# Performance work log

Measured on AMD Instinct MI355X. Metric: run time of the kernel, lower is better.

## Reference

```python
import jax, jax.numpy as jnp
import numpy as np

B, C, H, W = 32, 512, 32, 32
N = H * W            # seq_len = 1024
HEADS = 8
DH = C // HEADS      # 64
K = 256              # linformer low-rank
EPS = 1e-5


def setup_inputs() -> dict:
    key = jax.random.key(0)
    ks = jax.random.split(key, 10)
    s = 0.02
    return {
        "x": jax.random.normal(ks[0], (B, C, H, W), dtype=jnp.float32),
        "pos": jax.random.normal(ks[1], (1, N, C), dtype=jnp.float32),
        "ln_g": jnp.ones((C,), dtype=jnp.float32),
        "ln_b": jnp.zeros((C,), dtype=jnp.float32),
        "Wq": jax.random.normal(ks[2], (C, C), dtype=jnp.float32) * s,
        "Wk": jax.random.normal(ks[3], (C, C), dtype=jnp.float32) * s,
        "Wv": jax.random.normal(ks[4], (C, C), dtype=jnp.float32) * s,
        "proj_k": jax.random.normal(ks[5], (N, K), dtype=jnp.float32) * s,
        "proj_v": jax.random.normal(ks[6], (N, K), dtype=jnp.float32) * s,
        "Wo": jax.random.normal(ks[7], (C, C), dtype=jnp.float32) * s,
        "bo": jnp.zeros((C,), dtype=jnp.float32),
    }


def reference(x, pos, ln_g, ln_b, Wq, Wk, Wv, proj_k, proj_v, Wo, bo):
    b, c, h, w = x.shape
    n = h * w
    # b c h w -> b (h w) c
    xf = x.reshape(b, c, n).transpose(0, 2, 1) + pos
    # LayerNorm (biased variance, eps=1e-5) + ReLU; dropout = identity (eval)
    mu = xf.mean(-1, keepdims=True)
    var = jnp.var(xf, axis=-1, keepdims=True)
    y = (xf - mu) * jax.lax.rsqrt(var + EPS) * ln_g + ln_b
    y = jax.nn.relu(y)
    # Linformer self-attention
    q = y @ Wq                                   # [b,n,c]
    k_ = jnp.einsum('bnd,nk->bkd', y @ Wk, proj_k)  # [b,K,c]
    v_ = jnp.einsum('bnd,nk->bkd', y @ Wv, proj_v)  # [b,K,c]
    q = q.reshape(b, n, HEADS, DH)
    k_ = k_.reshape(b, K, HEADS, DH)
    v_ = v_.reshape(b, K, HEADS, DH)
    dots = jnp.einsum('bnhd,bkhd->bhnk', q, k_) * (DH ** -0.5)
    attn = jax.nn.softmax(dots, axis=-1)
    out = jnp.einsum('bhnk,bkhd->bnhd', attn, v_).reshape(b, n, c)
    out = out @ Wo + bo
    # residual with (x + pos), then back to b c h w
    out = out + xf
    return out.transpose(0, 2, 1).reshape(b, c, h, w)
```

## Files before the change

### kernel.cpp

```cpp
#include <hip/hip_runtime.h>
#include <hip/hip_bf16.h>
#include <cstdint>

#define BB  32
#define CC  512
#define NN  1024
#define HH  8
#define DHH 64
#define KR  256

using f32x4  = __attribute__((ext_vector_type(4))) float;
using f32x16 = __attribute__((ext_vector_type(16))) float;
using bf16x8 = __attribute__((ext_vector_type(8))) __bf16;
using u32x4  = __attribute__((ext_vector_type(4))) unsigned int;

__device__ __forceinline__ unsigned short f2bf(float f) {
  unsigned int u = __float_as_uint(f);
  u += 0x7fffu + ((u >> 16) & 1u);
  return (unsigned short)(u >> 16);
}

__device__ __forceinline__ float bf2f(unsigned short u) {
  return __uint_as_float(((unsigned int)u) << 16);
}

__device__ __forceinline__ unsigned int pknat(float a, float b) {
  unsigned short ua = __builtin_bit_cast(unsigned short, (__bf16)a);
  unsigned short ub = __builtin_bit_cast(unsigned short, (__bf16)b);
  return (unsigned int)ua | ((unsigned int)ub << 16);
}

__device__ __forceinline__ void gload16(const void* gsrc, void* ldst) {
  __builtin_amdgcn_global_load_lds(
      (const __attribute__((address_space(1))) unsigned int*)gsrc,
      (__attribute__((address_space(3))) unsigned int*)ldst, 16, 0, 0);
}

__global__ __launch_bounds__(256) void transcvt_all(
    const float* __restrict__ w0, const float* __restrict__ w1,
    const float* __restrict__ w2, const float* __restrict__ w3,
    const float* __restrict__ p0, const float* __restrict__ p1,
    const float* __restrict__ pos,
    unsigned short* __restrict__ d0, unsigned short* __restrict__ d1,
    unsigned short* __restrict__ d2, unsigned short* __restrict__ d3,
    unsigned short* __restrict__ e0, unsigned short* __restrict__ e1,
    float* __restrict__ posT) {
  const int m = blockIdx.y;
  int idx = blockIdx.x * 256 + threadIdx.x;
  if (m == 6) {
    #pragma unroll
    for (int h = 0; h < 2; ++h) {
      int e = idx + h * 262144;
      int c = e >> 10, n = e & 1023;
      posT[e] = pos[(size_t)n * CC + c];
    }
    return;
  }
  const float* src = m==0?w0:m==1?w1:m==2?w2:m==3?w3:m==4?p0:p1;
  unsigned short* dst = m==0?d0:m==1?d1:m==2?d2:m==3?d3:m==4?e0:e1;
  if (m < 4) {
    int dr = idx & 511;
    int dc = idx >> 9;
    dst[idx] = f2bf(src[(size_t)dr * 512 + dc]);
  } else {
    int n = idx & 1023, kk = idx >> 10;
    dst[idx] = f2bf(src[(size_t)n * 256 + kk]);
  }
}

__global__ __launch_bounds__(1024) void ln_relu_kernel(
    const float* __restrict__ x, const float* __restrict__ posT,
    const float* __restrict__ g, const float* __restrict__ bta,
    unsigned short* __restrict__ y, unsigned short* __restrict__ yT) {
  __shared__ unsigned short tile[512][68];
  __shared__ float smp[16][16][8];
  __shared__ float smu[64], srs[64];
  const int b = blockIdx.y, n0 = blockIdx.x * 64;
  const int tid = threadIdx.x;
  const int wv = tid >> 6, ln_ = tid & 63;
  const int q = tid & 15;
  const int rr = tid >> 4;
  const float* xb = x    + (size_t)b * CC * NN + n0 + q * 4;
  const float* pb = posT + n0 + q * 4;

  float4 xf[8];
  float s[4] = {0.f,0.f,0.f,0.f}, s2[4] = {0.f,0.f,0.f,0.f};
  #pragma unroll
  for (int hh = 0; hh < 2; ++hh) {
    float4 xv[4], pv[4];
    #pragma unroll
    for (int i = 0; i < 4; ++i) {
      const int c = rr + (hh * 4 + i) * 64;
      xv[i] = *reinterpret_cast<const float4*>(&xb[(size_t)c * NN]);
      pv[i] = *reinterpret_cast<const float4*>(&pb[(size_t)c * NN]);
    }
    #pragma unroll
    for (int i = 0; i < 4; ++i) {
      float4 f;
      f.x = xv[i].x + pv[i].x; f.y = xv[i].y + pv[i].y;
      f.z = xv[i].z + pv[i].z; f.w = xv[i].w + pv[i].w;
      s[0] += f.x; s2[0] += f.x * f.x;
      s[1] += f.y; s2[1] += f.y * f.y;
      s[2] += f.z; s2[2] += f.z * f.z;
      s[3] += f.w; s2[3] += f.w * f.w;
      xf[hh * 4 + i] = f;
    }
  }
  #pragma unroll
  for (int d = 16; d < 64; d <<= 1)
    #pragma unroll
    for (int k = 0; k < 4; ++k) {
      s[k]  += __shfl_xor(s[k],  d, 64);
      s2[k] += __shfl_xor(s2[k], d, 64);
    }
  if (ln_ < 16) {
    #pragma unroll
    for (int k = 0; k < 4; ++k) {
      smp[wv][ln_][k]     = s[k];
      smp[wv][ln_][k + 4] = s2[k];
    }
  }
  __syncthreads();

  if (tid < 64) {
    const int qq = tid >> 2, k = tid & 3;
    float ss = 0.f, ss2 = 0.f;
    #pragma unroll
    for (int w = 0; w < 16; ++w) { ss += smp[w][qq][k]; ss2 += smp[w][qq][k + 4]; }
    float mu = ss * (1.f / 512.f);
    float var = ss2 * (1.f / 512.f) - mu * mu;
    smu[tid] = mu;
    srs[tid] = rsqrtf(var + 1e-5f);
  }
  __syncthreads();

  {
    const float mu0 = smu[q * 4 + 0], rs0 = srs[q * 4 + 0];
    const float mu1 = smu[q * 4 + 1], rs1 = srs[q * 4 + 1];
    const float mu2 = smu[q * 4 + 2], rs2 = srs[q * 4 + 2];
    const float mu3 = smu[q * 4 + 3], rs3 = srs[q * 4 + 3];
    #pragma unroll
    for (int i = 0; i < 8; ++i) {
      const int c = rr + i * 64;
      const float gg = g[c], bb = bta[c];
      float o0 = (xf[i].x - mu0) * rs0 * gg + bb; o0 = o0 > 0.f ? o0 : 0.f;
      float o1 = (xf[i].y - mu1) * rs1 * gg + bb; o1 = o1 > 0.f ? o1 : 0.f;
      float o2 = (xf[i].z - mu2) * rs2 * gg + bb; o2 = o2 > 0.f ? o2 : 0.f;
      float o3 = (xf[i].w - mu3) * rs3 * gg + bb; o3 = o3 > 0.f ? o3 : 0.f;
      uint2 u; u.x = pknat(o0, o1); u.y = pknat(o2, o3);
      *reinterpret_cast<uint2*>(&tile[c][q * 4]) = u;
    }
  }
  __syncthreads();

  {
    const int tok = tid >> 4, seg = tid & 15;
    const int c0 = seg * 32;
    unsigned int pk16[16];
    #pragma unroll
    for (int cc = 0; cc < 32; cc += 2) {
      const int ccr = (cc + seg * 2) & 31;
      unsigned short v0 = tile[c0 + ccr][tok];
      unsigned short v1 = tile[c0 + ccr + 1][tok];
      pk16[ccr >> 1] = (unsigned int)v0 | ((unsigned int)v1 << 16);
    }
    unsigned short* yb = y + ((size_t)b * NN + n0 + tok) * CC + c0;
    #pragma unroll
    for (int v4 = 0; v4 < 4; ++v4) {
      uint4 w;
      w.x = pk16[v4 * 4 + 0]; w.y = pk16[v4 * 4 + 1];
      w.z = pk16[v4 * 4 + 2]; w.w = pk16[v4 * 4 + 3];
      *reinterpret_cast<uint4*>(&yb[v4 * 8]) = w;
    }
  }

  {
    const int c = tid & 511, hf = tid >> 9;
    const int toff = hf * 32;
    unsigned short* ytb = yT + (size_t)b * CC * NN + (size_t)c * NN + n0 + toff;
    #pragma unroll
    for (int v4 = 0; v4 < 4; ++v4) {
      uint2 a0 = *reinterpret_cast<const uint2*>(&tile[c][toff + v4 * 8]);
      uint2 a1 = *reinterpret_cast<const uint2*>(&tile[c][toff + v4 * 8 + 4]);
      uint4 w; w.x = a0.x; w.y = a0.y; w.z = a1.x; w.w = a1.y;
      *reinterpret_cast<uint4*>(&ytb[v4 * 8]) = w;
    }
  }
}

template <int MODE>
__global__ __launch_bounds__(256) void gemm_tn(
    const unsigned short* __restrict__ A, int lda, long long strideA,
    const unsigned short* __restrict__ Bt, int ldb, long long strideB,
    unsigned short* __restrict__ Cb, long long strideC,
    unsigned short* __restrict__ Cb2, long long strideC2,
    int Nn, int Kk, int TB,
    const float* __restrict__ xres, const float* __restrict__ posT,
    const float* __restrict__ bias, float* __restrict__ outF) {
  __shared__ __align__(16) unsigned short sh[24576];
  unsigned short* aL = sh;
  unsigned short* bL = sh + 12288;
  const int zb = blockIdx.z;
  int sel = 0, mb;
  if (MODE == 3) {
    sel = blockIdx.y >> 1;
    mb = ((blockIdx.y & 1) + sel * 2) * 128;
    if (sel == 1) Bt += (size_t)512 * 512;
  } else {
    mb = blockIdx.y * 128;
  }
  const int nb = blockIdx.x * 128;
  A  += (size_t)strideA * zb;
  Bt += (size_t)strideB * zb;
  Cb += (size_t)strideC * zb;
  if (MODE == 3) Cb2 += (size_t)strideC2 * zb;
  const int tid  = threadIdx.x;
  const int lane = tid & 63;
  const int wave = tid >> 6;
  const int wm = (wave >> 1) * 64, wn = (wave & 1) * 64;
  const int sr  = lane >> 2;
  const int scw = lane & 3;
  f32x4 acc[4][4] = {};

  auto stage = [&](int buf, int k0) {
    #pragma unroll
    for (int i = 0; i < 2; ++i) {
      int rbase = wave * 32 + i * 16;
      int row = rbase + sr;
      int ca = scw ^ ((row ^ (row >> 2)) & 3);
      gload16(&A [(size_t)(mb + row) * lda + k0 + ca * 8], &aL[buf * 4096 + rbase * 32]);
      gload16(&Bt[(size_t)(nb + row) * ldb + k0 + ca * 8], &bL[buf * 4096 + rbase * 32]);
    }
  };

  const int nt = Kk >> 5;
  stage(0, 0);
  stage(1, 32);
  asm volatile("s_waitcnt vmcnt(4)" ::: "memory");
  __builtin_amdgcn_s_barrier();
  __builtin_amdgcn_sched_barrier(0);

  int cbuf = 0;
  for (int t = 0; t < nt; ++t) {
    if (t + 2 < nt) stage(cbuf == 0 ? 2 : cbuf - 1, (t + 2) << 5);

    bf16x8 af[4], bfv[4];
    const int kc = lane >> 4;
    #pragma unroll
    for (int i = 0; i < 4; ++i) {
      int ra = wm + i * 16 + (lane & 15);
      int rb = wn + i * 16 + (lane & 15);
      af[i]  = *reinterpret_cast<const bf16x8*>(&aL[cbuf * 4096 + ra * 32 + (kc ^ ((ra ^ (ra >> 2)) & 3)) * 8]);
      bfv[i] = *reinterpret_cast<const bf16x8*>(&bL[cbuf * 4096 + rb * 32 + (kc ^ ((rb ^ (rb >> 2)) & 3)) * 8]);
    }
    #pragma unroll
    for (int i = 0; i < 4; ++i)
      #pragma unroll
      for (int j = 0; j < 4; ++j)
        acc[i][j] = __builtin_amdgcn_mfma_f32_16x16x32_bf16(af[i], bfv[j], acc[i][j], 0, 0, 0);

    if (t + 2 < nt)      { asm volatile("s_waitcnt vmcnt(4)" ::: "memory"); }
    else if (t + 1 < nt) { asm volatile("s_waitcnt vmcnt(0)" ::: "memory"); }
    if (t + 1 < nt) {
      __builtin_amdgcn_s_barrier();
      __builtin_amdgcn_sched_barrier(0);
    }
    cbuf = (cbuf == 2) ? 0 : cbuf + 1;
  }

  if (MODE == 2) {
    float* Ct = reinterpret_cast<float*>(sh);
    const int halfsel = wave >> 1;
    const int t0base = nb & 1023;
    const int bcell = nb >> 10;
    float4 xr[16];
    #pragma unroll
    for (int half = 0; half < 2; ++half)
      #pragma unroll
      for (int p8 = 0; p8 < 8; ++p8) {
        int e = p8 * 256 + tid;
        int r = e >> 5, f4 = (e & 31) * 4;
        int c = mb + half * 64 + r;
        xr[half * 8 + p8] = *reinterpret_cast<const float4*>(
            &xres[((size_t)bcell * CC + c) * NN + t0base + f4]);
      }
    #pragma unroll
    for (int half = 0; half < 2; ++half) {
      __syncthreads();
      if (halfsel == half) {
        #pragma unroll
        for (int i = 0; i < 4; ++i) {
          int rloc = i * 16 + ((lane >> 4) << 2);
          #pragma unroll
          for (int j = 0; j < 4; ++j) {
            int cl = wn + j * 16 + (lane & 15);
            #pragma unroll
            for (int t = 0; t < 4; ++t)
              Ct[(rloc + t) * 132 + cl] = acc[i][j][t];
          }
        }
      }
      __syncthreads();
      #pragma unroll
      for (int p8 = 0; p8 < 8; ++p8) {
        int e = p8 * 256 + tid;
        int r = e >> 5, f4 = (e & 31) * 4;
        int c = mb + half * 64 + r;
        size_t base = ((size_t)bcell * CC + c) * NN + t0base + f4;
        float4 cv = *reinterpret_cast<const float4*>(&Ct[r * 132 + f4]);
        float4 xv = xr[half * 8 + p8];
        float4 pv = *reinterpret_cast<const float4*>(&posT[(size_t)c * NN + t0base + f4]);
        float bc = bias[c];
        float4 ov;
        ov.x = cv.x + xv.x + pv.x + bc;
        ov.y = cv.y + xv.y + pv.y + bc;
        ov.z = cv.z + xv.z + pv.z + bc;
        ov.w = cv.w + xv.w + pv.w + bc;
        *reinterpret_cast<float4*>(&outF[base]) = ov;
      }
    }
  } else {
    const bool transp = (MODE == 1) || (MODE == 3 && sel == 1);
    auto Ct = (unsigned short (*)[136])sh;
    __syncthreads();
    #pragma unroll
    for (int i = 0; i < 4; ++i) {
      const int r0 = wm + i * 16 + ((lane >> 4) << 2);
      #pragma unroll
      for (int j = 0; j < 4; ++j) {
        const int cl = wn + j * 16 + (lane & 15);
        #pragma unroll
        for (int t = 0; t < 4; ++t) {
          if (!transp) Ct[r0 + t][cl] = f2bf(acc[i][j][t]);
          else         Ct[cl][r0 + t] = f2bf(acc[i][j][t]);
        }
      }
    }
    __syncthreads();
    const int rr = tid >> 4, ch = tid & 15;
    #pragma unroll
    for (int it = 0; it < 8; ++it) {
      const int r = it * 16 + rr;
      uint4 v = *reinterpret_cast<const uint4*>(&Ct[r][ch * 8]);
      if (!transp)
        *reinterpret_cast<uint4*>(&Cb[(size_t)(mb + r) * Nn + nb + ch * 8]) = v;
      else if (MODE == 1)
        *reinterpret_cast<uint4*>(&Cb[(size_t)(nb + r) * TB + mb + ch * 8]) = v;
      else
        *reinterpret_cast<uint4*>(&Cb2[(size_t)(nb + r) * TB + (mb - 256) + ch * 8]) = v;
    }
  }
}

__global__ __launch_bounds__(256, 2) void attn_kernel(
    const unsigned short* __restrict__ q,
    const unsigned short* __restrict__ kB,
    const unsigned short* __restrict__ vT,
    unsigned short* __restrict__ O) {
  __shared__ __align__(16) unsigned short smem[32768];
  const int wgid = blockIdx.x;
  const int grp  = wgid & 255;
  const int tg   = wgid >> 8;
  const int h = grp & 7, b = grp >> 3;
  const int wave = threadIdx.x >> 6, lane = threadIdx.x & 63;
  const int t32 = lane & 31, g2 = lane >> 5;
  const int tokb = tg * 128 + wave * 32;

  const unsigned short* qp = q + ((size_t)(b * NN + tokb + t32)) * CC + h * DHH + g2 * 8;
  bf16x8 qf[4];
  #pragma unroll
  for (int st = 0; st < 4; ++st)
    qf[st] = *reinterpret_cast<const bf16x8*>(qp + (size_t)st * 16);

  {
    const unsigned short* kb = kB + ((size_t)b * KR) * CC + h * DHH;
    const int r0w = wave * 64;
    #pragma unroll
    for (int i = 0; i < 8; ++i) {
      int row = r0w + i * 8 + (lane >> 3);
      int sc  = (lane & 7) ^ (row & 7);
      gload16(kb + (size_t)row * CC + sc * 8, &smem[(r0w + i * 8) * 64]);
    }
    const unsigned short* vb = vT + ((size_t)b * CC + h * DHH) * KR;
    const int v0w = wave * 16;
    #pragma unroll
    for (int i = 0; i < 8; ++i) {
      int row = v0w + i * 2 + (lane >> 5);
      int sc  = (lane & 31) ^ (row & 7);
      gload16(vb + (size_t)row * KR + sc * 8, &smem[16384 + (v0w + i * 2) * 256]);
    }
  }
  __syncthreads();

  f32x16 s8[8] = {};
  #pragma unroll
  for (int t8 = 0; t8 < 8; ++t8) {
    const int row = t8 * 32 + t32;
    #pragma unroll
    for (int st = 0; st < 4; ++st) {
      int ch = (2 * st + g2) ^ (row & 7);
      bf16x8 kf = *reinterpret_cast<const bf16x8*>(&smem[row * 64 + ch * 8]);
      s8[t8] = __builtin_amdgcn_mfma_f32_32x32x16_bf16(kf, qf[st], s8[t8], 0, 0, 0);
    }
  }

  float m = -1e30f;
  #pragma unroll
  for (int t8 = 0; t8 < 8; ++t8)
    #pragma unroll
    for (int r = 0; r < 16; ++r) m = fmaxf(m, s8[t8][r]);
  m = fmaxf(m, __shfl_xor(m, 32));
  const float cexp = 0.125f * 1.44269504088896f;
  float ls = 0.f;
  #pragma unroll
  for (int t8 = 0; t8 < 8; ++t8)
    #pragma unroll
    for (int r = 0; r < 16; ++r) {
      float p = __builtin_amdgcn_exp2f((s8[t8][r] - m) * cexp);
      s8[t8][r] = p;
      ls += p;
    }
  ls += __shfl_xor(ls, 32);
  float rinv = __builtin_amdgcn_rcpf(ls);

  f32x16 o0 = {}, o1 = {};
  #pragma unroll
  for (int t8 = 0; t8 < 8; ++t8) {
    unsigned int pkd[8];
    #pragma unroll
    for (int qq = 0; qq < 4; ++qq) {
      pkd[qq * 2 + 0] = pknat(s8[t8][4 * qq + 0], s8[t8][4 * qq + 1]);
      pkd[qq * 2 + 1] = pknat(s8[t8][4 * qq + 2], s8[t8][4 * qq + 3]);
    }
    #pragma unroll
    for (int a = 0; a < 2; ++a) {
      const int ks = t8 * 2 + a;
      unsigned int xe0 = pkd[4 * a + 0], xe1 = pkd[4 * a + 1];
      unsigned int xo0 = pkd[4 * a + 2], xo1 = pkd[4 * a + 3];
      unsigned int d0 = g2 ? __shfl_xor(xo0, 32) : xe0;
      unsigned int d1 = g2 ? __shfl_xor(xo1, 32) : xe1;
      unsigned int d2 = g2 ? xo0 : __shfl_xor(xe0, 32);
      unsigned int d3 = g2 ? xo1 : __shfl_xor(xe1, 32);
      u32x4 pv_ = {d0, d1, d2, d3};
      bf16x8 pa = __builtin_bit_cast(bf16x8, pv_);
      #pragma unroll
      for (int dt = 0; dt < 2; ++dt) {
        int row = dt * 32 + t32;
        int ch = (2 * ks + g2) ^ (row & 7);
        bf16x8 bv = *reinterpret_cast<const bf16x8*>(&smem[16384 + row * 256 + ch * 8]);
        if (dt == 0) o0 = __builtin_amdgcn_mfma_f32_32x32x16_bf16(pa, bv, o0, 0, 0, 0);
        else         o1 = __builtin_amdgcn_mfma_f32_32x32x16_bf16(pa, bv, o1, 0, 0, 0);
      }
    }
  }

  unsigned short* Ob = O + ((size_t)(b * NN + tokb)) * CC + h * DHH;
  #pragma unroll
  for (int r = 0; r < 16; ++r) {
    int tl = (r & 3) + 8 * (r >> 2) + 4 * g2;
    float rs = __shfl(rinv, tl);
    Ob[(size_t)tl * CC + t32]      = f2bf(o0[r] * rs);
    Ob[(size_t)tl * CC + 32 + t32] = f2bf(o1[r] * rs);
  }
}

extern "C" void kernel_launch(void* const* d_in, const int* in_sizes, int n_in,
                              void* d_out, int out_size, void* d_ws, size_t ws_size,
                              hipStream_t stream) {
  const float* x    = (const float*)d_in[0];
  const float* pos  = (const float*)d_in[1];
  const float* ln_g = (const float*)d_in[2];
  const float* ln_b = (const float*)d_in[3];
  const float* Wq   = (const float*)d_in[4];
  const float* Wk   = (const float*)d_in[5];
  const float* Wv   = (const float*)d_in[6];
  const float* pk   = (const float*)d_in[7];
  const float* pv   = (const float*)d_in[8];
  const float* Wo   = (const float*)d_in[9];
  const float* bo   = (const float*)d_in[10];
  float* out = (float*)d_out;

  unsigned short* ws = (unsigned short*)d_ws;
  size_t off = 0;
  auto alloc = [&](size_t elems) { unsigned short* p = ws + off; off += elems; return p; };
  unsigned short* WqT     = alloc(512 * 512);
  unsigned short* WkT     = alloc(512 * 512);
  unsigned short* WvT     = alloc(512 * 512);
  unsigned short* WoT     = alloc(512 * 512);
  unsigned short* projcat = alloc((size_t)512 * 1024);
  float*          posTb   = (float*)alloc((size_t)512 * 1024 * 2);
  unsigned short* yB      = alloc((size_t)32768 * 512);
  unsigned short* yT      = alloc((size_t)32 * 512 * 1024);
  unsigned short* qB      = alloc((size_t)32768 * 512);
  unsigned short* zB      = alloc((size_t)32 * 512 * 512);
  unsigned short* kBuf    = alloc((size_t)32 * 256 * 512);
  unsigned short* vTB     = alloc((size_t)32 * 512 * 256);
  unsigned short* OB      = alloc((size_t)32768 * 512);

  transcvt_all<<<dim3(1024, 7), 256, 0, stream>>>(
      Wq, Wk, Wv, Wo, pk, pv, pos,
      WqT, WkT, WvT, WoT, projcat, projcat + (size_t)256 * 1024, posTb);

  ln_relu_kernel<<<dim3(16, 32), 1024, 0, stream>>>(x, posTb, ln_g, ln_b, yB, yT);

  gemm_tn<0><<<dim3(4, 256), 256, 0, stream>>>(
      yB, 512, 0, WqT, 512, 0, qB, 0, nullptr, 0,
      512, 512, 0, nullptr, nullptr, nullptr, nullptr);

  gemm_tn<0><<<dim3(4, 4, 32), 256, 0, stream>>>(
      projcat, 1024, 0, yT, 1024, (long long)512 * 1024, zB, (long long)512 * 512,
      nullptr, 0, 512, 1024, 0, nullptr, nullptr, nullptr, nullptr);

  gemm_tn<3><<<dim3(4, 4, 32), 256, 0, stream>>>(
      zB, 512, (long long)512 * 512, WkT, 512, 0, kBuf, (long long)256 * 512,
      vTB, (long long)512 * 256, 512, 512, 256, nullptr, nullptr, nullptr, nullptr);

  attn_kernel<<<dim3(2048, 1, 1), 256, 0, stream>>>(qB, kBuf, vTB, OB);

  gemm_tn<2><<<dim3(256, 4), 256, 0, stream>>>(
      WoT, 512, 0, OB, 512, 0, nullptr, 0, nullptr, 0,
      32768, 512, 0, x, posTb, bo, out);
}
```

Baseline: 209.3 us.

## Split fused LayerNorm into separate stats and apply kernels

Replaces the single 1024-thread LayerNorm+ReLU kernel with a stats kernel that writes per-token mean and rstd to a workspace buffer, and an apply kernel that rereads x and pos, normalizes, writes yT directly, and transposes via a smaller LDS tile to write y. The goal is smaller blocks, less LDS and register pressure, and more blocks in flight for better latency hiding. The cost is reading the full x and pos inputs twice, plus an extra kernel launch and a stats round-trip through global memory.

```diff
diff --git a/kernel.cpp b/kernel.cpp
--- a/kernel.cpp
+++ b/kernel.cpp
@@ -18,10 +18,6 @@
   unsigned int u = __float_as_uint(f);
   u += 0x7fffu + ((u >> 16) & 1u);
   return (unsigned short)(u >> 16);
-}
-
-__device__ __forceinline__ float bf2f(unsigned short u) {
-  return __uint_as_float(((unsigned int)u) << 16);
 }
 
 __device__ __forceinline__ unsigned int pknat(float a, float b) {
@@ -68,42 +64,36 @@
   }
 }
 
-__global__ __launch_bounds__(1024) void ln_relu_kernel(
+__global__ __launch_bounds__(512) void ln_stats_kernel(
     const float* __restrict__ x, const float* __restrict__ posT,
-    const float* __restrict__ g, const float* __restrict__ bta,
-    unsigned short* __restrict__ y, unsigned short* __restrict__ yT) {
-  __shared__ unsigned short tile[512][68];
-  __shared__ float smp[16][16][8];
-  __shared__ float smu[64], srs[64];
-  const int b = blockIdx.y, n0 = blockIdx.x * 64;
+    float2* __restrict__ stats) {
+  __shared__ float smp[8][16][8];
+  const int b = blockIdx.x, n0 = blockIdx.y * 64;
   const int tid = threadIdx.x;
-  const int wv = tid >> 6, ln_ = tid & 63;
-  const int q = tid & 15;
-  const int rr = tid >> 4;
-  const float* xb = x    + (size_t)b * CC * NN + n0 + q * 4;
-  const float* pb = posT + n0 + q * 4;
-
-  float4 xf[8];
+  const int wv = tid >> 6, lane = tid & 63;
+  const int nq = tid & 15;
+  const int cg = tid >> 4;
+  const float* xb = x    + (size_t)b * CC * NN + n0 + nq * 4;
+  const float* pb = posT + n0 + nq * 4;
+
   float s[4] = {0.f,0.f,0.f,0.f}, s2[4] = {0.f,0.f,0.f,0.f};
   #pragma unroll
-  for (int hh = 0; hh < 2; ++hh) {
+  for (int hh = 0; hh < 4; ++hh) {
     float4 xv[4], pv[4];
     #pragma unroll
     for (int i = 0; i < 4; ++i) {
-      const int c = rr + (hh * 4 + i) * 64;
+      const int c = cg * 16 + hh * 4 + i;
       xv[i] = *reinterpret_cast<const float4*>(&xb[(size_t)c * NN]);
       pv[i] = *reinterpret_cast<const float4*>(&pb[(size_t)c * NN]);
     }
     #pragma unroll
     for (int i = 0; i < 4; ++i) {
-      float4 f;
-      f.x = xv[i].x + pv[i].x; f.y = xv[i].y + pv[i].y;
-      f.z = xv[i].z + pv[i].z; f.w = xv[i].w + pv[i].w;
-      s[0] += f.x; s2[0] += f.x * f.x;
-      s[1] += f.y; s2[1] += f.y * f.y;
-      s[2] += f.z; s2[2] += f.z * f.z;
-      s[3] += f.w; s2[3] += f.w * f.w;
-      xf[hh * 4 + i] = f;
+      float f0 = xv[i].x + pv[i].x, f1 = xv[i].y + pv[i].y;
+      float f2 = xv[i].z + pv[i].z, f3 = xv[i].w + pv[i].w;
+      s[0] += f0; s2[0] += f0 * f0;
+      s[1] += f1; s2[1] += f1 * f1;
+      s[2] += f2; s2[2] += f2 * f2;
+      s[3] += f3; s2[3] += f3 * f3;
     }
   }
   #pragma unroll
@@ -113,77 +103,84 @@
       s[k]  += __shfl_xor(s[k],  d, 64);
       s2[k] += __shfl_xor(s2[k], d, 64);
     }
-  if (ln_ < 16) {
+  if (lane < 16) {
     #pragma unroll
     for (int k = 0; k < 4; ++k) {
-      smp[wv][ln_][k]     = s[k];
-      smp[wv][ln_][k + 4] = s2[k];
+      smp[wv][lane][k]     = s[k];
+      smp[wv][lane][k + 4] = s2[k];
     }
   }
   __syncthreads();
-
   if (tid < 64) {
     const int qq = tid >> 2, k = tid & 3;
     float ss = 0.f, ss2 = 0.f;
     #pragma unroll
-    for (int w = 0; w < 16; ++w) { ss += smp[w][qq][k]; ss2 += smp[w][qq][k + 4]; }
+    for (int w = 0; w < 8; ++w) { ss += smp[w][qq][k]; ss2 += smp[w][qq][k + 4]; }
     float mu = ss * (1.f / 512.f);
     float var = ss2 * (1.f / 512.f) - mu * mu;
-    smu[tid] = mu;
-    srs[tid] = rsqrtf(var + 1e-5f);
+    float2 st; st.x = mu; st.y = rsqrtf(var + 1e-5f);
+    stats[(size_t)b * NN + n0 + tid] = st;
+  }
+}
+
+__global__ __launch_bounds__(256) void ln_apply_kernel(
+    const float* __restrict__ x, const float* __restrict__ posT,
+    const float2* __restrict__ stats,
+    const float* __restrict__ g, const float* __restrict__ bta,
+    unsigned short* __restrict__ y, unsigned short* __restrict__ yT) {
+  __shared__ unsigned short tile[64][258];
+  const int b = blockIdx.x, c0 = blockIdx.y * 64, n0 = blockIdx.z * 256;
+  const int tid = threadIdx.x;
+  const int nq = tid & 63;
+  const int cg = tid >> 6;
+  const int n4 = nq * 4;
+  const float* xb = x    + (size_t)b * CC * NN + n0 + n4;
+  const float* pb = posT + n0 + n4;
+
+  float mu[4], rs[4];
+  #pragma unroll
+  for (int j = 0; j < 4; ++j) {
+    float2 st = stats[(size_t)b * NN + n0 + n4 + j];
+    mu[j] = st.x; rs[j] = st.y;
+  }
+
+  #pragma unroll
+  for (int hh = 0; hh < 4; ++hh) {
+    float4 xv[4], pv[4];
+    #pragma unroll
+    for (int i = 0; i < 4; ++i) {
+      const int c = c0 + cg * 16 + hh * 4 + i;
+      xv[i] = *reinterpret_cast<const float4*>(&xb[(size_t)c * NN]);
+      pv[i] = *reinterpret_cast<const float4*>(&pb[(size_t)c * NN]);
+    }
+    #pragma unroll
+    for (int i = 0; i < 4; ++i) {
+      const int c = c0 + cg * 16 + hh * 4 + i;
+      const float gg = g[c], bb = bta[c];
+      float o0 = (xv[i].x + pv[i].x - mu[0]) * rs[0] * gg + bb; o0 = o0 > 0.f ? o0 : 0.f;
+      float o1 = (xv[i].y + pv[i].y - mu[1]) * rs[1] * gg + bb; o1 = o1 > 0.f ? o1 : 0.f;
+      float o2 = (xv[i].z + pv[i].z - mu[2]) * rs[2] * gg + bb; o2 = o2 > 0.f ? o2 : 0.f;
+      float o3 = (xv[i].w + pv[i].w - mu[3]) * rs[3] * gg + bb; o3 = o3 > 0.f ? o3 : 0.f;
+      uint2 u; u.x = pknat(o0, o1); u.y = pknat(o2, o3);
+      *reinterpret_cast<uint2*>(&yT[((size_t)b * CC + c) * NN + n0 + n4]) = u;
+      *reinterpret_cast<uint2*>(&tile[c - c0][n4]) = u;
+    }
   }
   __syncthreads();
 
   {
-    const float mu0 = smu[q * 4 + 0], rs0 = srs[q * 4 + 0];
-    const float mu1 = smu[q * 4 + 1], rs1 = srs[q * 4 + 1];
-    const float mu2 = smu[q * 4 + 2], rs2 = srs[q * 4 + 2];
-    const float mu3 = smu[q * 4 + 3], rs3 = srs[q * 4 + 3];
-    #pragma unroll
-    for (int i = 0; i < 8; ++i) {
-      const int c = rr + i * 64;
-      const float gg = g[c], bb = bta[c];
-      float o0 = (xf[i].x - mu0) * rs0 * gg + bb; o0 = o0 > 0.f ? o0 : 0.f;
-      float o1 = (xf[i].y - mu1) * rs1 * gg + bb; o1 = o1 > 0.f ? o1 : 0.f;
-      float o2 = (xf[i].z - mu2) * rs2 * gg + bb; o2 = o2 > 0.f ? o2 : 0.f;
-      float o3 = (xf[i].w - mu3) * rs3 * gg + bb; o3 = o3 > 0.f ? o3 : 0.f;
-      uint2 u; u.x = pknat(o0, o1); u.y = pknat(o2, o3);
-      *reinterpret_cast<uint2*>(&tile[c][q * 4]) = u;
-    }
-  }
-  __syncthreads();
-
-  {
-    const int tok = tid >> 4, seg = tid & 15;
-    const int c0 = seg * 32;
-    unsigned int pk16[16];
-    #pragma unroll
-    for (int cc = 0; cc < 32; cc += 2) {
-      const int ccr = (cc + seg * 2) & 31;
-      unsigned short v0 = tile[c0 + ccr][tok];
-      unsigned short v1 = tile[c0 + ccr + 1][tok];
-      pk16[ccr >> 1] = (unsigned int)v0 | ((unsigned int)v1 << 16);
-    }
-    unsigned short* yb = y + ((size_t)b * NN + n0 + tok) * CC + c0;
-    #pragma unroll
-    for (int v4 = 0; v4 < 4; ++v4) {
+    const int t = tid;
+    unsigned int pk[32];
+    #pragma unroll
+    for (int cc = 0; cc < 64; cc += 2)
+      pk[cc >> 1] = (unsigned int)tile[cc][t] | ((unsigned int)tile[cc + 1][t] << 16);
+    unsigned short* yb = y + ((size_t)b * NN + n0 + t) * CC + c0;
+    #pragma unroll
+    for (int v4 = 0; v4 < 8; ++v4) {
       uint4 w;
-      w.x = pk16[v4 * 4 + 0]; w.y = pk16[v4 * 4 + 1];
-      w.z = pk16[v4 * 4 + 2]; w.w = pk16[v4 * 4 + 3];
+      w.x = pk[v4 * 4 + 0]; w.y = pk[v4 * 4 + 1];
+      w.z = pk[v4 * 4 + 2]; w.w = pk[v4 * 4 + 3];
       *reinterpret_cast<uint4*>(&yb[v4 * 8]) = w;
-    }
-  }
-
-  {
-    const int c = tid & 511, hf = tid >> 9;
-    const int toff = hf * 32;
-    unsigned short* ytb = yT + (size_t)b * CC * NN + (size_t)c * NN + n0 + toff;
-    #pragma unroll
-    for (int v4 = 0; v4 < 4; ++v4) {
-      uint2 a0 = *reinterpret_cast<const uint2*>(&tile[c][toff + v4 * 8]);
-      uint2 a1 = *reinterpret_cast<const uint2*>(&tile[c][toff + v4 * 8 + 4]);
-      uint4 w; w.x = a0.x; w.y = a0.y; w.z = a1.x; w.w = a1.y;
-      *reinterpret_cast<uint4*>(&ytb[v4 * 8]) = w;
     }
   }
 }
@@ -489,6 +486,7 @@
   unsigned short* WoT     = alloc(512 * 512);
   unsigned short* projcat = alloc((size_t)512 * 1024);
   float*          posTb   = (float*)alloc((size_t)512 * 1024 * 2);
+  float2*         statsB  = (float2*)alloc((size_t)32 * 1024 * 4);
   unsigned short* yB      = alloc((size_t)32768 * 512);
   unsigned short* yT      = alloc((size_t)32 * 512 * 1024);
   unsigned short* qB      = alloc((size_t)32768 * 512);
@@ -501,7 +499,9 @@
       Wq, Wk, Wv, Wo, pk, pv, pos,
       WqT, WkT, WvT, WoT, projcat, projcat + (size_t)256 * 1024, posTb);
 
-  ln_relu_kernel<<<dim3(16, 32), 1024, 0, stream>>>(x, posTb, ln_g, ln_b, yB, yT);
+  ln_stats_kernel<<<dim3(32, 16), 512, 0, stream>>>(x, posTb, statsB);
+  ln_apply_kernel<<<dim3(32, 8, 4), 256, 0, stream>>>(
+      x, posTb, statsB, ln_g, ln_b, yB, yT);
 
   gemm_tn<0><<<dim3(4, 256), 256, 0, stream>>>(
       yB, 512, 0, WqT, 512, 0, qB, 0, nullptr, 0,
```

New measurement: 207.7 us. About the same (-0.7%).
